# Kernel optimization log

Measured on AMD Instinct MI355X. Metric: run time of the kernel, lower is better.

The kernel has to match this reference:

```python
import jax, jax.numpy as jnp
import numpy as np

N_PATCH = 676
K_SEL = int(676 * 0.8)  # 540
HEADS = 16
LN_EPS = 1e-5


def _layernorm(t, w, b):
    mu = t.mean(-1, keepdims=True)
    var = ((t - mu) ** 2).mean(-1, keepdims=True)
    return (t - mu) * jax.lax.rsqrt(var + LN_EPS) * w + b


def _attention(t, w_qkv, b_qkv, w_out, b_out):
    # t: [S, B, C] (seq-first, like torch nn.MultiheadAttention)
    S, B, C = t.shape
    D = C // HEADS
    qkv = t @ w_qkv.T + b_qkv                       # [S, B, 3C]
    q, k, v = jnp.split(qkv, 3, axis=-1)
    def heads(a):
        return a.reshape(S, B, HEADS, D).transpose(1, 2, 0, 3)  # [B,H,S,D]
    q, k, v = heads(q), heads(k), heads(v)
    scores = jnp.einsum('bhqd,bhkd->bhqk', q, k) / jnp.sqrt(jnp.asarray(D, t.dtype))
    attn = jax.nn.softmax(scores, axis=-1)
    o = jnp.einsum('bhqk,bhkd->bhqd', attn, v)      # [B,H,S,D]
    o = o.transpose(2, 0, 1, 3).reshape(S, B, C)
    return o @ w_out.T + b_out


def _mlp(t, w_fc1, b_fc1, w_fc2, b_fc2):
    h = t @ w_fc1.T + b_fc1
    h = h * jax.nn.sigmoid(1.702 * h)  # CLIP QuickGELU
    return h @ w_fc2.T + b_fc2


def setup_inputs() -> dict:
    key = jax.random.key(0)
    ks = jax.random.split(key, 6)
    C, B, L = 1024, 32, 77
    inp = {
        'x': jax.random.normal(ks[0], (1 + N_PATCH, B, C), jnp.float32),
        'lang_tokens': jax.random.normal(ks[1], (L, B, C), jnp.float32),
        'ln1_w': jnp.ones((C,), jnp.float32),
        'ln1_b': jnp.zeros((C,), jnp.float32),
        'ln2_w': jnp.ones((C,), jnp.float32),
        'ln2_b': jnp.zeros((C,), jnp.float32),
        'w_qkv': jax.random.normal(ks[2], (3 * C, C), jnp.float32) * 0.02,
        'b_qkv': jnp.zeros((3 * C,), jnp.float32),
        'w_out': jax.random.normal(ks[3], (C, C), jnp.float32) * 0.02,
        'b_out': jnp.zeros((C,), jnp.float32),
        'w_fc1': jax.random.normal(ks[4], (4 * C, C), jnp.float32) * 0.02,
        'b_fc1': jnp.zeros((4 * C,), jnp.float32),
        'w_fc2': jax.random.normal(ks[5], (C, 4 * C), jnp.float32) * 0.02,
        'b_fc2': jnp.zeros((C,), jnp.float32),
    }
    return inp


def reference(x, lang_tokens, ln1_w, ln1_b, ln2_w, ln2_b, w_qkv, b_qkv,
              w_out, b_out, w_fc1, b_fc1, w_fc2, b_fc2):
    Nfull, B, C = x.shape
    cls_x = x[:1]            # [1, B, C]
    xt = x[1:]               # [676, B, C]

    # per-token language-alignment score: [676, B]
    score = jnp.einsum('nbc,lbc->nbl', xt, lang_tokens).mean(-1)

    # top-k selection per batch column; torch boolean-mask gather preserves
    # the ORIGINAL token order within the high/low sets -> sort the indices.
    order = jnp.argsort(-score, axis=0)                 # descending
    high_idx = jnp.sort(order[:K_SEL], axis=0)          # [540, B]
    low_idx = jnp.sort(order[K_SEL:], axis=0)           # [136, B]

    delta_x = jnp.take_along_axis(xt, high_idx[:, :, None], axis=0)  # [540,B,C]
    low_x = jnp.take_along_axis(xt, low_idx[:, :, None], axis=0)     # [136,B,C]
    low_score = jnp.take_along_axis(score, low_idx, axis=0)[:, :, None]
    low_tok = (low_x * jax.nn.softmax(low_score, axis=0)).sum(0, keepdims=True)

    seq = jnp.concatenate([cls_x, delta_x, low_tok], axis=0)  # [542, B, C]
    d = _attention(_layernorm(seq, ln1_w, ln1_b), w_qkv, b_qkv, w_out, b_out)

    barange = jnp.arange(B)[None, :]
    temple = jnp.zeros_like(xt)
    temple = temple.at[high_idx, barange].set(d[1:-1])
    temple = temple.at[low_idx, barange].set(
        jnp.broadcast_to(d[-1:], (N_PATCH - K_SEL, B, C)))

    xt = xt + temple
    cls_x = cls_x + d[:1]
    x = jnp.concatenate([cls_x, xt], axis=0)
    x = x + _mlp(_layernorm(x, ln2_w, ln2_b), w_fc1, b_fc1, w_fc2, b_fc2)
    return x
```

## Files before the change

### kernel.cpp

```cpp
#include <hip/hip_runtime.h>
#include <hip/hip_bf16.h>

typedef unsigned short u16;
typedef __attribute__((ext_vector_type(4))) float f32x4;
typedef __attribute__((ext_vector_type(8))) short s16x8;

#define DEVI __device__ __forceinline__

static constexpr int NPATCH = 676;
static constexpr int KSEL   = 540;
static constexpr int NLOW   = 136;
static constexpr int BB     = 32;
static constexpr int CC     = 1024;
static constexpr int S      = 542;
static constexpr int SP     = 576;
static constexpr int M1P    = SP * BB;
static constexpr int NTOK   = 677;
static constexpr int M2     = NTOK * BB;
static constexpr int M2P    = 21760;
static constexpr int MHALF  = 10880;
static constexpr int NKT    = SP / 64;
static constexpr int NQC    = 5;

DEVI u16 f2bf(float f) {
  unsigned u = __float_as_uint(f);
  u += 0x7fffu + ((u >> 16) & 1u);
  return (u16)(u >> 16);
}
DEVI u16 f2bf_fast(float f) {
  __hip_bfloat16 h = __float2bfloat16(f);
  return *(u16*)&h;
}
DEVI float bf2f(u16 h) { return __uint_as_float(((unsigned)h) << 16); }
DEVI float ex2(float x) { float r; asm("v_exp_f32 %0, %1" : "=v"(r) : "v"(x)); return r; }

DEVI void gld16(const void* g, void* l) {
  __builtin_amdgcn_global_load_lds((const __attribute__((address_space(1))) void*)g,
                                   (__attribute__((address_space(3))) void*)l,
                                   16, 0, 0);
}

DEVI void BAR() {
  asm volatile("" ::: "memory");
  __builtin_amdgcn_s_barrier();
  asm volatile("" ::: "memory");
}
#define VMC(N) asm volatile("s_waitcnt vmcnt(" #N ")" ::: "memory")


__global__ void k_wconv(const float* __restrict__ s0, const float* __restrict__ s1,
                        const float* __restrict__ s2, const float* __restrict__ s3,
                        u16* __restrict__ out) {
  int i = blockIdx.x * blockDim.x + threadIdx.x;
  const float* src;
  long off;
  if (i < 786432)       { src = s0; off = 0; }
  else if (i < 1048576) { src = s1; off = 786432; }
  else if (i < 2097152) { src = s2; off = 1048576; }
  else                  { src = s3; off = 2097152; }
  float4 v = ((const float4*)src)[i - off];
  unsigned long long p = (unsigned long long)f2bf(v.x)
                       | ((unsigned long long)f2bf(v.y) << 16)
                       | ((unsigned long long)f2bf(v.z) << 32)
                       | ((unsigned long long)f2bf(v.w) << 48);
  *(unsigned long long*)&out[(long)i * 4] = p;
}

__global__ void k_langmean(const float* __restrict__ lang, float* __restrict__ lm) {
  int b = blockIdx.x, t = threadIdx.x;
  float a0 = 0, a1 = 0, a2 = 0, a3 = 0;
  for (int l = 0; l < 77; l++) {
    float4 v = ((const float4*)(lang + ((long)l * BB + b) * CC))[t];
    a0 += v.x; a1 += v.y; a2 += v.z; a3 += v.w;
  }
  const float inv = 1.f / 77.f;
  float4 o; o.x = a0 * inv; o.y = a1 * inv; o.z = a2 * inv; o.w = a3 * inv;
  ((float4*)(lm + b * CC))[t] = o;
}

__global__ void k_score(const float* __restrict__ x, const float* __restrict__ lm,
                        float* __restrict__ score) {
  int nb = blockIdx.x;
  int n = nb >> 5, b = nb & 31;
  int t = threadIdx.x;
  float4 xv = ((const float4*)(x + ((long)(n + 1) * BB + b) * CC))[t];
  float4 lv = ((const float4*)(lm + b * CC))[t];
  float s = xv.x * lv.x + xv.y * lv.y + xv.z * lv.z + xv.w * lv.w;
  for (int m = 1; m < 64; m <<= 1) s += __shfl_xor(s, m);
  __shared__ float sm[4];
  if ((t & 63) == 0) sm[t >> 6] = s;
  __syncthreads();
  if (t == 0) score[n * BB + b] = sm[0] + sm[1] + sm[2] + sm[3];
}

__global__ void k_select(const float* __restrict__ score, float* __restrict__ wall,
                         int* __restrict__ rowmap, int* __restrict__ selsrc,
                         int* __restrict__ lowlist) {
  int b = blockIdx.x, t = threadIdx.x;
  __shared__ float sc[NPATCH];
  __shared__ int hf[NPATCH];
  __shared__ float red[2];
  if (t < NPATCH) sc[t] = score[t * BB + b];
  __syncthreads();
  int high = 0;
  if (t < NPATCH) {
    float s = sc[t];
    int r = 0;
    for (int m = 0; m < NPATCH; m++) {
      float sm_ = sc[m];
      r += (sm_ > s) || (sm_ == s && m < t);
    }
    high = (r < KSEL);
    hf[t] = high;
  }
  __syncthreads();
  if (t < NPATCH) {
    int p = 0;
    for (int m = 0; m < t; m++) p += hf[m];
    if (high) {
      rowmap[b * NPATCH + t] = 1 + p;
      selsrc[b * S + 1 + p] = t + 1;
    } else {
      rowmap[b * NPATCH + t] = S - 1;
      lowlist[b * NLOW + (t - p)] = t;
    }
  }
  if (t == 0) selsrc[b * S + 0] = 0;
  __syncthreads();
  if (t == 0) {
    float m = -3e38f;
    for (int i = 0; i < NPATCH; i++) if (!hf[i]) m = fmaxf(m, sc[i]);
    float d = 0;
    for (int i = 0; i < NPATCH; i++) if (!hf[i]) d += __expf(sc[i] - m);
    red[0] = m; red[1] = d;
  }
  __syncthreads();
  if (t < NPATCH) wall[b * NPATCH + t] = hf[t] ? 0.f : __expf(sc[t] - red[0]) / red[1];
}

__global__ void k_lowtok(const float* __restrict__ x, const float* __restrict__ wall,
                         const int* __restrict__ lowlist, float* __restrict__ lowtok) {
  int b = blockIdx.x, ch = blockIdx.y;
  int c = ch * 256 + threadIdx.x;
  float acc = 0.f;
  for (int i = 0; i < NLOW; i++) {
    int n = lowlist[b * NLOW + i];
    acc += wall[b * NPATCH + n] * x[((long)(n + 1) * BB + b) * CC + c];
  }
  lowtok[b * CC + c] = acc;
}

__global__ void k_lnseq(const float* __restrict__ x, const float* __restrict__ lowtok,
                        const int* __restrict__ selsrc, const float* __restrict__ w,
                        const float* __restrict__ bias, u16* __restrict__ out) {
  int s = blockIdx.x, b = blockIdx.y, t = threadIdx.x;
  u16* orow = out + ((long)b * SP + s) * CC;
  if (s >= S) { *(unsigned long long*)&orow[4 * t] = 0ULL; return; }
  const float* src;
  if (s == 0)          src = x + (long)b * CC;
  else if (s == S - 1) src = lowtok + (long)b * CC;
  else                 src = x + ((long)selsrc[b * S + s] * BB + b) * CC;
  float4 v = ((const float4*)src)[t];
  float ss = v.x + v.y + v.z + v.w;
  float s2 = v.x * v.x + v.y * v.y + v.z * v.z + v.w * v.w;
  for (int k = 1; k < 64; k <<= 1) { ss += __shfl_xor(ss, k); s2 += __shfl_xor(s2, k); }
  __shared__ float sa[4], sb[4];
  if ((t & 63) == 0) { sa[t >> 6] = ss; sb[t >> 6] = s2; }
  __syncthreads();
  ss = sa[0] + sa[1] + sa[2] + sa[3];
  s2 = sb[0] + sb[1] + sb[2] + sb[3];
  float mu = ss * (1.f / CC);
  float var = s2 * (1.f / CC) - mu * mu;
  float rs = rsqrtf(var + 1e-5f);
  int c = 4 * t;
  unsigned long long p = (unsigned long long)f2bf((v.x - mu) * rs * w[c]     + bias[c])
                       | ((unsigned long long)f2bf((v.y - mu) * rs * w[c + 1] + bias[c + 1]) << 16)
                       | ((unsigned long long)f2bf((v.z - mu) * rs * w[c + 2] + bias[c + 2]) << 32)
                       | ((unsigned long long)f2bf((v.w - mu) * rs * w[c + 3] + bias[c + 3]) << 48);
  *(unsigned long long*)&orow[4 * t] = p;
}

__global__ void k_scatln(const float* __restrict__ x, const u16* __restrict__ dbuf,
                         const int* __restrict__ rowmap, const float* __restrict__ w,
                         const float* __restrict__ bias, float* __restrict__ out,
                         u16* __restrict__ lnout) {
  int m = blockIdx.x, t = threadIdx.x;
  u16* orow = lnout + (long)m * CC;
  if (m >= M2) { *(unsigned long long*)&orow[4 * t] = 0ULL; return; }
  int nf = m >> 5, b = m & 31;
  int srow = (nf == 0) ? 0 : rowmap[b * NPATCH + (nf - 1)];
  float4 xv = ((const float4*)(x + (long)m * CC))[t];
  unsigned long long dp = *(const unsigned long long*)&dbuf[((long)b * SP + srow) * CC + 4 * t];
  float4 v;
  v.x = xv.x + bf2f((u16)(dp));
  v.y = xv.y + bf2f((u16)(dp >> 16));
  v.z = xv.z + bf2f((u16)(dp >> 32));
  v.w = xv.w + bf2f((u16)(dp >> 48));
  ((float4*)(out + (long)m * CC))[t] = v;
  float ss = v.x + v.y + v.z + v.w;
  float s2 = v.x * v.x + v.y * v.y + v.z * v.z + v.w * v.w;
  for (int k = 1; k < 64; k <<= 1) { ss += __shfl_xor(ss, k); s2 += __shfl_xor(s2, k); }
  __shared__ float sa[4], sb[4];
  if ((t & 63) == 0) { sa[t >> 6] = ss; sb[t >> 6] = s2; }
  __syncthreads();
  ss = sa[0] + sa[1] + sa[2] + sa[3];
  s2 = sb[0] + sb[1] + sb[2] + sb[3];
  float mu = ss * (1.f / CC);
  float var = s2 * (1.f / CC) - mu * mu;
  float rs = rsqrtf(var + 1e-5f);
  int c = 4 * t;
  unsigned long long p = (unsigned long long)f2bf((v.x - mu) * rs * w[c]     + bias[c])
                       | ((unsigned long long)f2bf((v.y - mu) * rs * w[c + 1] + bias[c + 1]) << 16)
                       | ((unsigned long long)f2bf((v.z - mu) * rs * w[c + 2] + bias[c + 2]) << 32)
                       | ((unsigned long long)f2bf((v.w - mu) * rs * w[c + 3] + bias[c + 3]) << 48);
  *(unsigned long long*)&orow[4 * t] = p;
}


struct Epi {
  const float* bias;
  u16* obf;
  float* of;
  u16 *qb, *kb, *vtb;
  int mvalid, ldc;
};

DEVI void stage32(u16* dst, const u16* src, int ld) {
  int t = threadIdx.x;
#pragma unroll
  for (int q = 0; q < 2; q++) {
    int s = t + q * 256;
    int R = s >> 3, clp = s & 7;
    int lc = clp ^ (R & 7);
    int m = 2 * R + (lc >> 2), kc = lc & 3;
    gld16(src + (long)m * ld + kc * 8, dst + s * 8);
  }
}

DEVI s16x8 frag32(const u16* tile, int m, int h4) {
  int R = m >> 1;
  int phys = ((((m & 1) << 2) | h4) ^ (R & 7));
  return *(const s16x8*)(tile + R * 64 + phys * 8);
}

DEVI void stage64(u16* dst, const u16* src, int ld) {
  int t = threadIdx.x;
  int c = t & 7, r0 = t >> 3;
  gld16(src + (long)r0 * ld + ((c ^ (r0 & 7)) << 3), dst + t * 8);
  int r1 = r0 + 32;
  gld16(src + (long)r1 * ld + ((c ^ (r1 & 7)) << 3), dst + 2048 + t * 8);
}

DEVI s16x8 frag(const u16* half, int rh, int kk, int h4) {
  int chunk = ((kk << 2) | h4) ^ (rh & 7);
  return *(const s16x8*)(half + rh * 64 + chunk * 8);
}

template<int MODE>
DEVI void epi_store(const Epi& e, int m0, int n, const f32x4& a, float bias) {
  const float QSC = 0.125f * 1.44269504088896f;
  if (MODE == 0) {
    int part = n >> 10, cc = n & 1023;
    int hh = cc >> 6, dd = cc & 63;
    int b0 = m0 / SP, s0 = m0 % SP;
    if (part == 2) {
      u16 pk[4];
#pragma unroll
      for (int tt = 0; tt < 4; tt++) pk[tt] = f2bf(a[tt] + bias);
      *(unsigned long long*)&e.vtb[((long)(b0 * 16 + hh) * 64 + dd) * SP + s0] =
          *(unsigned long long*)pk;
    } else {
      u16* dst = (part == 0 ? e.qb : e.kb) + ((long)(b0 * 16 + hh) * SP + s0) * 64 + dd;
      float scl = (part == 0) ? QSC : 1.f;
#pragma unroll
      for (int tt = 0; tt < 4; tt++) dst[tt * 64] = f2bf((a[tt] + bias) * scl);
    }
  } else if (MODE == 1) {
#pragma unroll
    for (int tt = 0; tt < 4; tt++)
      e.obf[(long)(m0 + tt) * e.ldc + n] = f2bf(a[tt] + bias);
  } else if (MODE == 2) {
#pragma unroll
    for (int tt = 0; tt < 4; tt++) {
      float v = a[tt] + bias;
      v = v / (1.f + __expf(-1.702f * v));
      e.obf[(long)(m0 + tt) * e.ldc + n] = f2bf(v);
    }
  } else {
#pragma unroll
    for (int tt = 0; tt < 4; tt++) {
      int m = m0 + tt;
      if (m < e.mvalid) e.of[(long)m * CC + n] += a[tt] + bias;
    }
  }
}


template<int MODE>
__global__ __launch_bounds__(256, 3) void k_gemm5(const u16* __restrict__ A, int lda,
                                                  const u16* __restrict__ Bw, int ldb,
                                                  int K, Epi e) {
  __shared__ __align__(16) u16 lds[3][2][4096];
  int t = threadIdx.x;
  int lane = t & 63, w = t >> 6;
  int h4 = lane >> 4, r = lane & 15;
  int wr = w >> 1, wc = w & 1;
  int MBk = gridDim.x, NBk = gridDim.y;
  int nwg = MBk * NBk;
  int orig = blockIdx.y * MBk + blockIdx.x;
  int q8 = nwg >> 3, r8 = nwg & 7, xcd = orig & 7, rk = orig >> 3;
  int wgid = (xcd < r8 ? xcd * (q8 + 1) : r8 * (q8 + 1) + (xcd - r8) * q8) + rk;
  int bm = wgid / NBk, bn = wgid % NBk;

  const u16* Asrc = A + (long)bm * 128 * lda;
  const u16* Bsrc = Bw + (long)bn * 128 * ldb;
  int NT = K >> 5;

  f32x4 acc[4][4];
#pragma unroll
  for (int i = 0; i < 4; i++)
#pragma unroll
    for (int j = 0; j < 4; j++) acc[i][j] = {0.f, 0.f, 0.f, 0.f};

  stage32(lds[0][0], Asrc, lda);
  stage32(lds[0][1], Bsrc, ldb);
  if (NT > 1) {
    stage32(lds[1][0], Asrc + 32, lda);
    stage32(lds[1][1], Bsrc + 32, ldb);
  }

  int bufr = 0, bufw = 2;
  for (int kt = 0; kt < NT; kt++) {
    if (kt + 1 < NT) { VMC(4); } else { VMC(0); }
    BAR();
    if (kt + 2 < NT) {
      stage32(lds[bufw][0], Asrc + (kt + 2) * 32, lda);
      stage32(lds[bufw][1], Bsrc + (kt + 2) * 32, ldb);
    }
    const u16* At = lds[bufr][0];
    const u16* Bt = lds[bufr][1];
    s16x8 af[4], bf[4];
#pragma unroll
    for (int i = 0; i < 4; i++) af[i] = frag32(At, wr * 64 + i * 16 + r, h4);
#pragma unroll
    for (int j = 0; j < 4; j++) bf[j] = frag32(Bt, wc * 64 + j * 16 + r, h4);
#pragma unroll
    for (int i = 0; i < 4; i++)
#pragma unroll
      for (int j = 0; j < 4; j++)
        acc[i][j] = __builtin_amdgcn_mfma_f32_16x16x32_bf16(af[i], bf[j], acc[i][j], 0, 0, 0);
    bufr = (bufr == 2) ? 0 : bufr + 1;
    bufw = (bufw == 2) ? 0 : bufw + 1;
  }

#pragma unroll
  for (int i = 0; i < 4; i++) {
    int m0 = bm * 128 + wr * 64 + i * 16 + 4 * h4;
#pragma unroll
    for (int j = 0; j < 4; j++) {
      int n = bn * 128 + wc * 64 + j * 16 + r;
      float bias = (MODE == 3 && e.bias == nullptr) ? 0.f : e.bias[n];
      epi_store<MODE>(e, m0, n, acc[i][j], bias);
    }
  }
}


template<int MODE>
__global__ __launch_bounds__(256, 2) void k_gemm7(const u16* __restrict__ A, int lda,
                                                  const u16* __restrict__ Bw, int ldb,
                                                  int K, Epi e) {
  __shared__ __align__(16) u16 lds[3][3][4096];
  int t = threadIdx.x;
  int lane = t & 63, w = t >> 6;
  int h4 = lane >> 4, r = lane & 15;
  int wr = w >> 1, wc = w & 1;
  int MBk = gridDim.x, NBk = gridDim.y;
  int nwg = MBk * NBk;
  int orig = blockIdx.y * MBk + blockIdx.x;
  int q8 = nwg >> 3, r8 = nwg & 7, xcd = orig & 7, rk = orig >> 3;
  int wgid = (xcd < r8 ? xcd * (q8 + 1) : r8 * (q8 + 1) + (xcd - r8) * q8) + rk;
  int bm = wgid / NBk, bn = wgid % NBk;

  const u16* Asrc = A + (long)bm * 128 * lda;
  const u16* Bsrc = Bw + (long)bn * 256 * ldb;
  int NT = K >> 5;

  f32x4 acc[4][8];
#pragma unroll
  for (int i = 0; i < 4; i++)
#pragma unroll
    for (int j = 0; j < 8; j++) acc[i][j] = {0.f, 0.f, 0.f, 0.f};

  stage32(lds[0][0], Asrc, lda);
  stage32(lds[0][1], Bsrc, ldb);
  stage32(lds[0][2], Bsrc + (long)128 * ldb, ldb);
  if (NT > 1) {
    stage32(lds[1][0], Asrc + 32, lda);
    stage32(lds[1][1], Bsrc + 32, ldb);
    stage32(lds[1][2], Bsrc + (long)128 * ldb + 32, ldb);
  }

  int bufr = 0, bufw = 2;
  for (int kt = 0; kt < NT; kt++) {
    if (kt + 1 < NT) { VMC(6); } else { VMC(0); }
    BAR();
    if (kt + 2 < NT) {
      stage32(lds[bufw][0], Asrc + (kt + 2) * 32, lda);
      stage32(lds[bufw][1], Bsrc + (kt + 2) * 32, ldb);
      stage32(lds[bufw][2], Bsrc + (long)128 * ldb + (kt + 2) * 32, ldb);
    }
    const u16* At = lds[bufr][0];
    const u16* Bt = lds[bufr][1 + wc];
    s16x8 af[4], bf[8];
#pragma unroll
    for (int i = 0; i < 4; i++) af[i] = frag32(At, wr * 64 + i * 16 + r, h4);
#pragma unroll
    for (int j = 0; j < 8; j++) bf[j] = frag32(Bt, j * 16 + r, h4);
#pragma unroll
    for (int i = 0; i < 4; i++)
#pragma unroll
      for (int j = 0; j < 8; j++)
        acc[i][j] = __builtin_amdgcn_mfma_f32_16x16x32_bf16(af[i], bf[j], acc[i][j], 0, 0, 0);
    bufr = (bufr == 2) ? 0 : bufr + 1;
    bufw = (bufw == 2) ? 0 : bufw + 1;
  }

#pragma unroll
  for (int i = 0; i < 4; i++) {
    int m0 = bm * 128 + wr * 64 + i * 16 + 4 * h4;
#pragma unroll
    for (int j = 0; j < 8; j++) {
      int n = bn * 256 + wc * 128 + j * 16 + r;
      float bias = (MODE == 3 && e.bias == nullptr) ? 0.f : e.bias[n];
      epi_store<MODE>(e, m0, n, acc[i][j], bias);
    }
  }
}


__global__ __launch_bounds__(256, 4) void k_attn2(const u16* __restrict__ qb,
                                                  const u16* __restrict__ kb,
                                                  const u16* __restrict__ vtb,
                                                  u16* __restrict__ aout) {
  __shared__ __align__(16) u16 Kt[2][4096];
  __shared__ __align__(16) u16 Vt[2][4096];
  __shared__ __align__(16) u16 Pl[4][1024];

  int nwg = gridDim.x;
  int orig = blockIdx.x;
  int q8 = nwg >> 3, r8 = nwg & 7, xcd = orig & 7, rk = orig >> 3;
  int wgid = (xcd < r8 ? xcd * (q8 + 1) : r8 * (q8 + 1) + (xcd - r8) * q8) + rk;
  int bh = wgid / NQC, qc = wgid % NQC;
  int b = bh >> 4, hh = bh & 15;
  int t = threadIdx.x, w = t >> 6, lane = t & 63;
  int h4 = lane >> 4, r = lane & 15;

  const u16* Q  = qb  + (long)bh * SP * 64;
  const u16* Kg = kb  + (long)bh * SP * 64;
  const u16* Vg = vtb + (long)bh * 64 * SP;

  s16x8 ones;
#pragma unroll
  for (int j = 0; j < 8; j++) ones[j] = (short)0x3F80;

  int qt[2];
  bool act[2];
  s16x8 aq0[2], aq1[2];
  f32x4 o[2][4];
  f32x4 ls[2];
  float mM[2][4];
#pragma unroll
  for (int sub = 0; sub < 2; sub++) {
    qt[sub] = qc * 8 + w * 2 + sub;
    act[sub] = qt[sub] < SP / 16;
    if (act[sub]) {
      aq0[sub] = *(const s16x8*)&Q[(qt[sub] * 16 + r) * 64 + h4 * 8];
      aq1[sub] = *(const s16x8*)&Q[(qt[sub] * 16 + r) * 64 + 32 + h4 * 8];
    }
    ls[sub] = {0.f, 0.f, 0.f, 0.f};
#pragma unroll
    for (int i = 0; i < 4; i++) { o[sub][i] = {0.f, 0.f, 0.f, 0.f}; mM[sub][i] = -1e30f; }
  }

  stage64(Kt[0], Kg, 64);
  stage64(Vt[0], Vg, SP);
  VMC(0);
  BAR();

  for (int kt = 0; kt < NKT; kt++) {
    int cur = kt & 1;
    if (kt + 1 < NKT) {
      stage64(Kt[cur ^ 1], Kg + (kt + 1) * 64 * 64, 64);
      stage64(Vt[cur ^ 1], Vg + (kt + 1) * 64, SP);
    }
    int kv0 = kt * 64;
    const u16* Kc = Kt[cur];
    const u16* Vc = Vt[cur];
#pragma unroll
    for (int sub = 0; sub < 2; sub++) {
      if (!act[sub]) continue;
      f32x4 sf[4];
#pragma unroll
      for (int f = 0; f < 4; f++) {
        sf[f] = {0.f, 0.f, 0.f, 0.f};
        sf[f] = __builtin_amdgcn_mfma_f32_16x16x32_bf16(aq0[sub], frag(Kc, f * 16 + r, 0, h4), sf[f], 0, 0, 0);
        sf[f] = __builtin_amdgcn_mfma_f32_16x16x32_bf16(aq1[sub], frag(Kc, f * 16 + r, 1, h4), sf[f], 0, 0, 0);
      }
      if (kv0 + 64 > S) {
#pragma unroll
        for (int f = 0; f < 4; f++)
          if (kv0 + f * 16 + r >= S) {
#pragma unroll
            for (int tt = 0; tt < 4; tt++) sf[f][tt] = -1e30f;
          }
      }
      float mxl[4];
#pragma unroll
      for (int tt = 0; tt < 4; tt++)
        mxl[tt] = fmaxf(fmaxf(sf[0][tt], sf[1][tt]), fmaxf(sf[2][tt], sf[3][tt]));
      int need = 0;
#pragma unroll
      for (int tt = 0; tt < 4; tt++) need |= (mxl[tt] > mM[sub][tt] + 8.f);
      if (__any(need)) {
        for (int msk = 1; msk < 16; msk <<= 1) {
#pragma unroll
          for (int tt = 0; tt < 4; tt++) mxl[tt] = fmaxf(mxl[tt], __shfl_xor(mxl[tt], msk));
        }
#pragma unroll
        for (int tt = 0; tt < 4; tt++) {
          float mn = fmaxf(mM[sub][tt], mxl[tt]);
          float sc = ex2(mM[sub][tt] - mn);
          mM[sub][tt] = mn;
          ls[sub][tt] *= sc;
#pragma unroll
          for (int nf = 0; nf < 4; nf++) o[sub][nf][tt] *= sc;
        }
      }
#pragma unroll
      for (int tt = 0; tt < 4; tt++) {
        float m_ = mM[sub][tt];
        sf[0][tt] = ex2(sf[0][tt] - m_);
        sf[1][tt] = ex2(sf[1][tt] - m_);
        sf[2][tt] = ex2(sf[2][tt] - m_);
        sf[3][tt] = ex2(sf[3][tt] - m_);
      }
      u16* Pw = Pl[w];
#pragma unroll
      for (int f = 0; f < 4; f++)
#pragma unroll
        for (int tt = 0; tt < 4; tt++) {
          int q = 4 * h4 + tt;
          int chunk = (f * 2 + (r >> 3)) ^ (q & 7);
          Pw[q * 64 + chunk * 8 + (r & 7)] = f2bf_fast(sf[f][tt]);
        }
      s16x8 pa0 = frag(Pw, r, 0, h4);
      s16x8 pa1 = frag(Pw, r, 1, h4);
#pragma unroll
      for (int nf = 0; nf < 4; nf++) {
        o[sub][nf] = __builtin_amdgcn_mfma_f32_16x16x32_bf16(pa0, frag(Vc, nf * 16 + r, 0, h4), o[sub][nf], 0, 0, 0);
        o[sub][nf] = __builtin_amdgcn_mfma_f32_16x16x32_bf16(pa1, frag(Vc, nf * 16 + r, 1, h4), o[sub][nf], 0, 0, 0);
      }
      ls[sub] = __builtin_amdgcn_mfma_f32_16x16x32_bf16(pa0, ones, ls[sub], 0, 0, 0);
      ls[sub] = __builtin_amdgcn_mfma_f32_16x16x32_bf16(pa1, ones, ls[sub], 0, 0, 0);
    }
    VMC(0);
    BAR();
  }

#pragma unroll
  for (int sub = 0; sub < 2; sub++) {
    if (!act[sub]) continue;
    float inv[4];
#pragma unroll
    for (int tt = 0; tt < 4; tt++) inv[tt] = 1.f / ls[sub][tt];
#pragma unroll
    for (int nf = 0; nf < 4; nf++)
#pragma unroll
      for (int tt = 0; tt < 4; tt++) {
        int q = qt[sub] * 16 + 4 * h4 + tt;
        if (q < S) aout[((long)b * SP + q) * CC + hh * 64 + nf * 16 + r] = f2bf_fast(o[sub][nf][tt] * inv[tt]);
      }
  }
}


extern "C" void kernel_launch(void* const* d_in, const int* in_sizes, int n_in,
                              void* d_out, int out_size, void* d_ws, size_t ws_size,
                              hipStream_t stream) {
  const float* x    = (const float*)d_in[0];
  const float* lang = (const float*)d_in[1];
  const float* ln1w = (const float*)d_in[2];
  const float* ln1b = (const float*)d_in[3];
  const float* ln2w = (const float*)d_in[4];
  const float* ln2b = (const float*)d_in[5];
  const float* wqkv = (const float*)d_in[6];
  const float* bqkv = (const float*)d_in[7];
  const float* wout = (const float*)d_in[8];
  const float* bout = (const float*)d_in[9];
  const float* wfc1 = (const float*)d_in[10];
  const float* bfc1 = (const float*)d_in[11];
  const float* wfc2 = (const float*)d_in[12];
  const float* bfc2 = (const float*)d_in[13];
  float* out = (float*)d_out;
  char* ws = (char*)d_ws;
  const size_t MiB = 1ull << 20;

  float* lm      = (float*)(ws + 0 * MiB);
  float* score   = (float*)(ws + 1 * MiB);
  float* wall    = (float*)(ws + 2 * MiB);
  int*   rowmap  = (int*)  (ws + 3 * MiB);
  int*   selsrc  = (int*)  (ws + 4 * MiB);
  int*   lowlist = (int*)  (ws + 5 * MiB);
  float* lowtok  = (float*)(ws + 6 * MiB);
  u16* wqb  = (u16*)(ws + 7 * MiB);
  u16* wob  = (u16*)(ws + 13 * MiB);
  u16* wf1b = (u16*)(ws + 15 * MiB);
  u16* wf2b = (u16*)(ws + 23 * MiB);
  u16* qbuf = (u16*)(ws + 31 * MiB);
  u16* kbuf = (u16*)(ws + 67 * MiB);
  u16* vtb  = (u16*)(ws + 103 * MiB);
  u16* regA = (u16*)(ws + 139 * MiB);
  u16* lnseq = regA;
  u16* aout  = regA;
  u16* dbuf  = vtb;
  u16* ln2bf = qbuf;
  u16* hbuf  = (u16*)(ws + 74 * MiB);

  k_wconv<<<3145728 / 256, 256, 0, stream>>>(wqkv, wout, wfc1, wfc2, wqb);

  k_langmean<<<BB, 256, 0, stream>>>(lang, lm);
  k_score<<<NPATCH * BB, 256, 0, stream>>>(x, lm, score);
  k_select<<<BB, 1024, 0, stream>>>(score, wall, rowmap, selsrc, lowlist);
  k_lowtok<<<dim3(BB, 4), 256, 0, stream>>>(x, wall, lowlist, lowtok);
  k_lnseq<<<dim3(SP, BB), 256, 0, stream>>>(x, lowtok, selsrc, ln1w, ln1b, lnseq);

  {
    Epi e = {};
    e.bias = bqkv; e.qb = qbuf; e.kb = kbuf; e.vtb = vtb; e.mvalid = M1P;
    k_gemm7<0><<<dim3(M1P / 128, 3072 / 256), 256, 0, stream>>>(lnseq, 1024, wqb, 1024, 1024, e);
  }

  k_attn2<<<BB * 16 * NQC, 256, 0, stream>>>(qbuf, kbuf, vtb, aout);

  {
    Epi e = {};
    e.bias = bout; e.obf = dbuf; e.mvalid = M1P; e.ldc = 1024;
    k_gemm5<1><<<dim3(M1P / 128, 1024 / 128), 256, 0, stream>>>(aout, 1024, wob, 1024, 1024, e);
  }

  k_scatln<<<M2P, 256, 0, stream>>>(x, dbuf, rowmap, ln2w, ln2b, out, ln2bf);

  for (int mc = 0; mc < 2; mc++) {
    int rvalid = (mc == 0) ? MHALF : (M2 - MHALF);
    Epi e2 = {};
    e2.bias = bfc1; e2.obf = hbuf; e2.mvalid = MHALF; e2.ldc = 4096;
    k_gemm7<2><<<dim3(MHALF / 128, 4096 / 256), 256, 0, stream>>>(
        ln2bf + (long)mc * MHALF * 1024, 1024, wf1b, 1024, 1024, e2);
    Epi e3 = {};
    e3.bias = bfc2; e3.of = out + (long)mc * MHALF * CC; e3.mvalid = rvalid;
    k_gemm5<3><<<dim3(MHALF / 128, 1024 / 128), 256, 0, stream>>>(
        hbuf, 4096, wf2b, 4096, 4096, e3);
  }
}
```

Before: 1.006 ms.

## Add 256x256-tile 8-wave GEMM for FC2 and rebalance MLP row chunks

Adds a new GEMM kernel with 512 threads and 256x256 output tiles. It uses double-buffered LDS and interleaves staging of A/B halves with MFMA phases, using s_setprio and explicit lgkmcnt waits. The kernel is used for the FC2 projection (K=4096) in place of the 128x128 gemm5. The MLP row split changes from two equal halves to 10752/11008 rows so each chunk is a multiple of 256. Larger tiles cut global and LDS traffic per FLOP, at the cost of fewer workgroups (168 per chunk) and higher register pressure.

```diff
diff --git a/kernel.cpp b/kernel.cpp
--- a/kernel.cpp
+++ b/kernel.cpp
@@ -18,7 +18,6 @@
 static constexpr int NTOK   = 677;
 static constexpr int M2     = NTOK * BB;
 static constexpr int M2P    = 21760;
-static constexpr int MHALF  = 10880;
 static constexpr int NKT    = SP / 64;
 static constexpr int NQC    = 5;
 
@@ -45,6 +44,8 @@
   __builtin_amdgcn_s_barrier();
   asm volatile("" ::: "memory");
 }
+#define LGKM0() do { asm volatile("s_waitcnt lgkmcnt(0)" ::: "memory"); \
+                     __builtin_amdgcn_sched_barrier(0); } while (0)
 #define VMC(N) asm volatile("s_waitcnt vmcnt(" #N ")" ::: "memory")
 
 
@@ -243,17 +244,26 @@
   return *(const s16x8*)(tile + R * 64 + phys * 8);
 }
 
+DEVI void stage_half(u16* dst, const u16* src, int ld) {
+  int t = threadIdx.x;
+  int c = t & 7;
+  int r0 = t >> 3;
+  gld16(src + (long)r0 * ld + ((c ^ (r0 & 7)) << 3), dst + (t << 3));
+  int r1 = r0 + 64;
+  gld16(src + (long)r1 * ld + ((c ^ (r1 & 7)) << 3), dst + 4096 + (t << 3));
+}
+
+DEVI s16x8 frag(const u16* half, int rh, int kk, int h4) {
+  int chunk = ((kk << 2) | h4) ^ (rh & 7);
+  return *(const s16x8*)(half + rh * 64 + chunk * 8);
+}
+
 DEVI void stage64(u16* dst, const u16* src, int ld) {
   int t = threadIdx.x;
   int c = t & 7, r0 = t >> 3;
   gld16(src + (long)r0 * ld + ((c ^ (r0 & 7)) << 3), dst + t * 8);
   int r1 = r0 + 32;
   gld16(src + (long)r1 * ld + ((c ^ (r1 & 7)) << 3), dst + 2048 + t * 8);
-}
-
-DEVI s16x8 frag(const u16* half, int rh, int kk, int h4) {
-  int chunk = ((kk << 2) | h4) ^ (rh & 7);
-  return *(const s16x8*)(half + rh * 64 + chunk * 8);
 }
 
 template<int MODE>
@@ -432,6 +442,143 @@
 #pragma unroll
     for (int j = 0; j < 8; j++) {
       int n = bn * 256 + wc * 128 + j * 16 + r;
+      float bias = (MODE == 3 && e.bias == nullptr) ? 0.f : e.bias[n];
+      epi_store<MODE>(e, m0, n, acc[i][j], bias);
+    }
+  }
+}
+
+
+template<int MODE>
+__global__ __launch_bounds__(512, 2) void k_gemm8(const u16* __restrict__ A, int lda,
+                                                  const u16* __restrict__ Bw, int ldb,
+                                                  int K, Epi e) {
+  __shared__ __align__(16) u16 lds[2][2][2][8192];
+  int t = threadIdx.x;
+  int lane = t & 63, w = t >> 6;
+  int h4 = lane >> 4, r = lane & 15;
+  int wr = w >> 2, wc = w & 3;
+  int MBk = gridDim.x, NBk = gridDim.y;
+  int nwg = MBk * NBk;
+  int orig = blockIdx.y * MBk + blockIdx.x;
+  int q8 = nwg >> 3, r8 = nwg & 7, xcd = orig & 7, rk = orig >> 3;
+  int wgid = (xcd < r8 ? xcd * (q8 + 1) : r8 * (q8 + 1) + (xcd - r8) * q8) + rk;
+  int bm = wgid / NBk, bn = wgid % NBk;
+
+  const u16* Asrc = A + (long)bm * 256 * lda;
+  const u16* Bsrc = Bw + (long)bn * 256 * ldb;
+  int NT = K >> 6;
+
+  f32x4 acc[8][4];
+#pragma unroll
+  for (int i = 0; i < 8; i++)
+#pragma unroll
+    for (int j = 0; j < 4; j++) acc[i][j] = {0.f, 0.f, 0.f, 0.f};
+
+  stage_half(lds[0][0][0], Asrc, lda);
+  stage_half(lds[0][0][1], Asrc + (long)128 * lda, lda);
+  stage_half(lds[0][1][0], Bsrc, ldb);
+  stage_half(lds[0][1][1], Bsrc + (long)128 * ldb, ldb);
+  {
+    const u16* B1 = Bsrc + (NT > 1 ? 64 : 0);
+    stage_half(lds[1][1][0], B1, ldb);
+    stage_half(lds[1][1][1], B1 + (long)128 * ldb, ldb);
+  }
+  VMC(4);
+  BAR();
+
+  for (int kt = 0; kt < NT; kt++) {
+    int buf = kt & 1;
+    const u16* Ah = lds[buf][0][wr];
+    const u16* Bh = lds[buf][1][wc >> 1];
+    int rbB = (wc & 1) << 6;
+    int ka = (kt + 1 < NT) ? kt + 1 : NT - 1;
+    int kb = (kt + 2 < NT) ? kt + 2 : NT - 1;
+    const u16* Aps = Asrc + ka * 64;
+    const u16* Bps = Bsrc + kb * 64;
+    u16* AdL = lds[(kt + 1) & 1][0][0];
+    u16* AdH = lds[(kt + 1) & 1][0][1];
+    u16* BdL = lds[buf][1][0];
+    u16* BdH = lds[buf][1][1];
+
+    s16x8 a8[8], b8[8];
+#pragma unroll
+    for (int i = 0; i < 4; i++) {
+      a8[i * 2]     = frag(Ah, i * 16 + r, 0, h4);
+      a8[i * 2 + 1] = frag(Ah, i * 16 + r, 1, h4);
+    }
+#pragma unroll
+    for (int j = 0; j < 2; j++) {
+      b8[j * 2]     = frag(Bh, rbB + j * 16 + r, 0, h4);
+      b8[j * 2 + 1] = frag(Bh, rbB + j * 16 + r, 1, h4);
+    }
+    stage_half(AdL, Aps, lda);
+    BAR(); LGKM0();
+    __builtin_amdgcn_s_setprio(1);
+#pragma unroll
+    for (int i = 0; i < 4; i++)
+#pragma unroll
+      for (int j = 0; j < 2; j++) {
+        acc[i][j] = __builtin_amdgcn_mfma_f32_16x16x32_bf16(a8[i * 2],     b8[j * 2],     acc[i][j], 0, 0, 0);
+        acc[i][j] = __builtin_amdgcn_mfma_f32_16x16x32_bf16(a8[i * 2 + 1], b8[j * 2 + 1], acc[i][j], 0, 0, 0);
+      }
+    __builtin_amdgcn_s_setprio(0);
+    BAR();
+#pragma unroll
+    for (int j = 0; j < 2; j++) {
+      b8[4 + j * 2]     = frag(Bh, rbB + (j + 2) * 16 + r, 0, h4);
+      b8[4 + j * 2 + 1] = frag(Bh, rbB + (j + 2) * 16 + r, 1, h4);
+    }
+    stage_half(AdH, Aps + (long)128 * lda, lda);
+    BAR(); LGKM0();
+    __builtin_amdgcn_s_setprio(1);
+#pragma unroll
+    for (int i = 0; i < 4; i++)
+#pragma unroll
+      for (int j = 0; j < 2; j++) {
+        acc[i][j + 2] = __builtin_amdgcn_mfma_f32_16x16x32_bf16(a8[i * 2],     b8[4 + j * 2],     acc[i][j + 2], 0, 0, 0);
+        acc[i][j + 2] = __builtin_amdgcn_mfma_f32_16x16x32_bf16(a8[i * 2 + 1], b8[4 + j * 2 + 1], acc[i][j + 2], 0, 0, 0);
+      }
+    __builtin_amdgcn_s_setprio(0);
+    BAR();
+#pragma unroll
+    for (int i = 0; i < 4; i++) {
+      a8[i * 2]     = frag(Ah, (i + 4) * 16 + r, 0, h4);
+      a8[i * 2 + 1] = frag(Ah, (i + 4) * 16 + r, 1, h4);
+    }
+    stage_half(BdL, Bps, ldb);
+    BAR(); LGKM0();
+    __builtin_amdgcn_s_setprio(1);
+#pragma unroll
+    for (int i = 0; i < 4; i++)
+#pragma unroll
+      for (int j = 0; j < 2; j++) {
+        acc[i + 4][j] = __builtin_amdgcn_mfma_f32_16x16x32_bf16(a8[i * 2],     b8[j * 2],     acc[i + 4][j], 0, 0, 0);
+        acc[i + 4][j] = __builtin_amdgcn_mfma_f32_16x16x32_bf16(a8[i * 2 + 1], b8[j * 2 + 1], acc[i + 4][j], 0, 0, 0);
+      }
+    __builtin_amdgcn_s_setprio(0);
+    BAR();
+    stage_half(BdH, Bps + (long)128 * ldb, ldb);
+    BAR();
+    __builtin_amdgcn_s_setprio(1);
+#pragma unroll
+    for (int i = 0; i < 4; i++)
+#pragma unroll
+      for (int j = 0; j < 2; j++) {
+        acc[i + 4][j + 2] = __builtin_amdgcn_mfma_f32_16x16x32_bf16(a8[i * 2],     b8[4 + j * 2],     acc[i + 4][j + 2], 0, 0, 0);
+        acc[i + 4][j + 2] = __builtin_amdgcn_mfma_f32_16x16x32_bf16(a8[i * 2 + 1], b8[4 + j * 2 + 1], acc[i + 4][j + 2], 0, 0, 0);
+      }
+    __builtin_amdgcn_s_setprio(0);
+    VMC(4);
+    BAR();
+  }
+
+#pragma unroll
+  for (int i = 0; i < 8; i++) {
+    int m0 = bm * 256 + wr * 128 + i * 16 + 4 * h4;
+#pragma unroll
+    for (int j = 0; j < 4; j++) {
+      int n = bn * 256 + wc * 64 + j * 16 + r;
       float bias = (MODE == 3 && e.bias == nullptr) ? 0.f : e.bias[n];
       epi_store<MODE>(e, m0, n, acc[i][j], bias);
     }
@@ -651,15 +798,22 @@
 
   k_scatln<<<M2P, 256, 0, stream>>>(x, dbuf, rowmap, ln2w, ln2b, out, ln2bf);
 
-  for (int mc = 0; mc < 2; mc++) {
-    int rvalid = (mc == 0) ? MHALF : (M2 - MHALF);
-    Epi e2 = {};
-    e2.bias = bfc1; e2.obf = hbuf; e2.mvalid = MHALF; e2.ldc = 4096;
-    k_gemm7<2><<<dim3(MHALF / 128, 4096 / 256), 256, 0, stream>>>(
-        ln2bf + (long)mc * MHALF * 1024, 1024, wf1b, 1024, 1024, e2);
-    Epi e3 = {};
-    e3.bias = bfc2; e3.of = out + (long)mc * MHALF * CC; e3.mvalid = rvalid;
-    k_gemm5<3><<<dim3(MHALF / 128, 1024 / 128), 256, 0, stream>>>(
-        hbuf, 4096, wf2b, 4096, 4096, e3);
-  }
-}
+  {
+    const int mrows[2] = {10752, 11008};
+    long moff = 0;
+    for (int mc = 0; mc < 2; mc++) {
+      int rows = mrows[mc];
+      Epi e2 = {};
+      e2.bias = bfc1; e2.obf = hbuf; e2.mvalid = rows; e2.ldc = 4096;
+      k_gemm7<2><<<dim3(rows / 128, 4096 / 256), 256, 0, stream>>>(
+          ln2bf + moff * 1024, 1024, wf1b, 1024, 1024, e2);
+      Epi e3 = {};
+      e3.bias = bfc2; e3.of = out + moff * CC;
+      int rem = M2 - (int)moff;
+      e3.mvalid = (rem < rows) ? rem : rows;
+      k_gemm8<3><<<dim3(rows / 256, 1024 / 256), 512, 0, stream>>>(
+          hbuf, 4096, wf2b, 4096, 4096, e3);
+      moff += rows;
+    }
+  }
+}
```

New measurement: 1.034 ms. +2.8%, slower.
